# Optimization experiments

Hardware: AMD Instinct MI355X
Metric: run time of the kernel (lower is better)

Reference implementation:

```python
import jax, jax.numpy as jnp
import numpy as np

N_NODES = 100000
FEAT = 256
EMBED = 128
K = 10          # sampled neighbors per node (num_sample)
E = 4096        # edge batch
NUM_CLASSES = 2


def setup_inputs() -> dict:
    key = jax.random.key(0)
    ks = jax.random.split(key, 6)
    edges = jax.random.randint(ks[0], (E, 2), 0, N_NODES)
    neigh_idx = jax.random.randint(ks[1], (N_NODES, K), 0, N_NODES)
    features = jax.random.normal(ks[2], (N_NODES, FEAT), dtype=jnp.float32)
    W1 = jax.random.normal(ks[3], (EMBED, FEAT), dtype=jnp.float32) * (FEAT ** -0.5)
    W2 = jax.random.normal(ks[4], (EMBED, EMBED), dtype=jnp.float32) * (EMBED ** -0.5)
    Wc = jax.random.normal(ks[5], (NUM_CLASSES, EMBED), dtype=jnp.float32) * (EMBED ** -0.5)
    return {"edges": edges, "neigh_idx": neigh_idx, "features": features,
            "W1": W1, "W2": W2, "Wc": Wc}


def reference(edges, neigh_idx, features, W1, W2, Wc):
    # 2-layer GraphSage-style encoder (gcn mean aggregation), batched over E edges.
    idx2 = neigh_idx[edges]              # [E,2,K]   1-hop neighbors of edge endpoints
    idx1 = neigh_idx[idx2]               # [E,2,K,K] 2-hop neighbors
    # layer 1: mean of raw features over 2-hop neighbor sets, then linear + relu
    f1 = jnp.mean(features[idx1], axis=3)                 # [E,2,K,FEAT]
    h1 = jax.nn.relu(jnp.einsum('epkf,df->epkd', f1, W1)) # [E,2,K,EMBED]
    # layer 2: mean over 1-hop neighbors, then linear (last encoder: no relu)
    h1m = jnp.mean(h1, axis=2)                            # [E,2,EMBED]
    h2 = jnp.einsum('epd,gd->epg', h1m, W2)               # [E,2,EMBED]
    # edge pooling ('mean'): average the two endpoint embeddings
    pooled = 0.5 * (h2[:, 0] + h2[:, 1])                  # [E,EMBED]
    # classifier: weight.mm(embeds).t()
    return pooled @ Wc.T                                  # [E,NUM_CLASSES]
```

## Files before the change

kernel.cpp:

```cpp
#include <hip/hip_runtime.h>
#include <hip/hip_bf16.h>


typedef __bf16 bf16x8 __attribute__((ext_vector_type(8)));
typedef float f32x4 __attribute__((ext_vector_type(4)));

#define FEAT 256
#define EMB  128
#define KNB  10
#define BM   128

__device__ inline unsigned short f2b(float f) {
  unsigned int u = __float_as_uint(f);
  unsigned int r = (u + 0x7fffu + ((u >> 16) & 1u)) >> 16;
  return (unsigned short)r;
}
__device__ inline float b2f(unsigned int s) {
  return __uint_as_float(s << 16);
}


__global__ __launch_bounds__(512, 4) void gemm_z(
    const float* __restrict__ feat, const float* __restrict__ W1,
    const float* __restrict__ W2, const float* __restrict__ Wc,
    unsigned short* __restrict__ z, float* __restrict__ M2, int M) {
  __shared__ unsigned short As[BM][FEAT + 8];

  if (blockIdx.x == gridDim.x - 1) {
    int t = threadIdx.x;
    if (t < 256) {
      int c = t >> 7, d = t & 127;
      float s = 0.f;
      for (int g = 0; g < EMB; ++g) s += Wc[c * EMB + g] * W2[g * EMB + d];
      M2[t] = s;
    }
    return;
  }

  const int wid  = threadIdx.x >> 6;
  const int lane = threadIdx.x & 63;
  const int m0   = blockIdx.x * BM;

  bf16x8 bfrag[8];
  {
    const int col = wid * 16 + (lane & 15);
    const int kof = (lane >> 4) * 8;
#pragma unroll
    for (int kk = 0; kk < 8; ++kk) {
      const float* src = &W1[col * FEAT + kk * 32 + kof];
      float4 lo = *reinterpret_cast<const float4*>(src);
      float4 hi = *reinterpret_cast<const float4*>(src + 4);
      union { unsigned short s[8]; bf16x8 v; } cvt;
      cvt.s[0] = f2b(lo.x); cvt.s[1] = f2b(lo.y); cvt.s[2] = f2b(lo.z); cvt.s[3] = f2b(lo.w);
      cvt.s[4] = f2b(hi.x); cvt.s[5] = f2b(hi.y); cvt.s[6] = f2b(hi.z); cvt.s[7] = f2b(hi.w);
      bfrag[kk] = cvt.v;
    }
  }

  const float4* f4 = reinterpret_cast<const float4*>(feat);
  for (int i = threadIdx.x; i < BM * 64; i += 512) {
    int r = i >> 6, c4 = i & 63;
    int row = m0 + r;
    float4 v = make_float4(0.f, 0.f, 0.f, 0.f);
    if (row < M) v = f4[(size_t)row * 64 + c4];
    ushort4 bq;
    bq.x = f2b(v.x); bq.y = f2b(v.y); bq.z = f2b(v.z); bq.w = f2b(v.w);
    *reinterpret_cast<ushort4*>(&As[r][c4 * 4]) = bq;
  }
  __syncthreads();

  f32x4 acc[BM / 16] = {};
  const int arow = lane & 15;
  const int kof  = (lane >> 4) * 8;
#pragma unroll
  for (int mt = 0; mt < BM / 16; ++mt) {
#pragma unroll
    for (int kk = 0; kk < 8; ++kk) {
      bf16x8 a = *reinterpret_cast<const bf16x8*>(&As[mt * 16 + arow][kk * 32 + kof]);
      acc[mt] = __builtin_amdgcn_mfma_f32_16x16x32_bf16(a, bfrag[kk], acc[mt], 0, 0, 0);
    }
  }

  const int col = wid * 16 + (lane & 15);
#pragma unroll
  for (int mt = 0; mt < BM / 16; ++mt) {
    int rbase = m0 + mt * 16 + (lane >> 4) * 4;
#pragma unroll
    for (int r = 0; r < 4; ++r) {
      int row = rbase + r;
      if (row < M) z[(size_t)row * EMB + col] = f2b(acc[mt][r]);
    }
  }
}


__global__ __launch_bounds__(128) void aggregate(
    const int* __restrict__ edges, const int* __restrict__ nidx,
    const unsigned short* __restrict__ z, const float* __restrict__ M2,
    float* __restrict__ out, int E) {
  __shared__ int   s_idx2[2][KNB];
  __shared__ int   s_idx1[2][KNB * KNB];
  __shared__ float s_pm[2][EMB];

  const int e = blockIdx.x;
  const int t = threadIdx.x;
  const int w = t >> 6;
  const int l = t & 63;
  const int h = l >> 5;
  const int q = l & 31;

  if (t < 2 * KNB) {
    int p = t / KNB, k = t % KNB;
    int v = edges[e * 2 + p];
    s_idx2[p][k] = nidx[(size_t)v * KNB + k];
  }
  __syncthreads();
  for (int i = t; i < 2 * KNB * KNB; i += 128) {
    int p = i / 100, r = i % 100;
    s_idx1[p][r] = nidx[(size_t)s_idx2[p][r / KNB] * KNB + (r % KNB)];
  }
  __syncthreads();

  float pooled[4] = {0.f, 0.f, 0.f, 0.f};
#pragma unroll
  for (int k = 0; k < KNB; ++k) {
    float a[4] = {0.f, 0.f, 0.f, 0.f};
#pragma unroll
    for (int jp = 0; jp < KNB / 2; ++jp) {
      int u = s_idx1[w][k * KNB + jp * 2 + h];
      uint2 v = *reinterpret_cast<const uint2*>(&z[(size_t)u * EMB + q * 4]);
      a[0] += b2f(v.x & 0xffffu); a[1] += b2f(v.x >> 16);
      a[2] += b2f(v.y & 0xffffu); a[3] += b2f(v.y >> 16);
    }
#pragma unroll
    for (int c = 0; c < 4; ++c) {
      float s = a[c] + __shfl_xor(a[c], 32);
      pooled[c] += fmaxf(s * 0.1f, 0.f);
    }
  }
  if (h == 0) {
#pragma unroll
    for (int c = 0; c < 4; ++c) s_pm[w][q * 4 + c] = pooled[c] * 0.1f;
  }
  __syncthreads();

  if (w == 0) {
    int d0 = 2 * l, d1 = 2 * l + 1;
    float p0 = 0.5f * (s_pm[0][d0] + s_pm[1][d0]);
    float p1 = 0.5f * (s_pm[0][d1] + s_pm[1][d1]);
    float s0 = p0 * M2[d0]       + p1 * M2[d1];
    float s1 = p0 * M2[EMB + d0] + p1 * M2[EMB + d1];
#pragma unroll
    for (int off = 32; off > 0; off >>= 1) {
      s0 += __shfl_down(s0, off);
      s1 += __shfl_down(s1, off);
    }
    if (l == 0) { out[e * 2 + 0] = s0; out[e * 2 + 1] = s1; }
  }
}


extern "C" void kernel_launch(void* const* d_in, const int* in_sizes, int n_in,
                              void* d_out, int out_size, void* d_ws, size_t ws_size,
                              hipStream_t stream) {
  const int*   edges = (const int*)d_in[0];
  const int*   nidx  = (const int*)d_in[1];
  const float* feat  = (const float*)d_in[2];
  const float* W1    = (const float*)d_in[3];
  const float* W2    = (const float*)d_in[4];
  const float* Wc    = (const float*)d_in[5];
  float* out = (float*)d_out;

  const int N = in_sizes[2] / FEAT;
  const int E = in_sizes[0] / 2;

  char* ws = (char*)d_ws;
  unsigned short* z = (unsigned short*)ws;
  float* M2 = (float*)(ws + (size_t)N * EMB * sizeof(unsigned short));

  int mtiles = (N + BM - 1) / BM;
  gemm_z <<<mtiles + 1, 512, 0, stream>>>(feat, W1, W2, Wc, z, M2, N);
  aggregate<<<E, 128, 0, stream>>>(edges, nidx, z, M2, out, E);
}
```

Before: 211.2 us.

## Pre-convert features and W1 to swizzled bf16, load tiles via async global-to-LDS

Adds a separate conversion kernel that writes features (XOR-swizzled by row) and W1 as bf16 into workspace and computes the Wc·W2 product. The GEMM then pulls its A tile straight into LDS with global_load_lds and reads it with a matching swizzle, using a smaller 64-row tile. The aim is to remove conversion work and register staging from the GEMM and avoid LDS bank conflicts, but it adds a full bf16 write and re-read of the feature matrix plus an extra launch.

```diff
diff --git a/kernel.cpp b/kernel.cpp
--- a/kernel.cpp
+++ b/kernel.cpp
@@ -8,7 +8,7 @@
 #define FEAT 256
 #define EMB  128
 #define KNB  10
-#define BM   128
+#define BM   64
 
 __device__ inline unsigned short f2b(float f) {
   unsigned int u = __float_as_uint(f);
@@ -19,72 +19,99 @@
   return __uint_as_float(s << 16);
 }
 
-
-__global__ __launch_bounds__(512, 4) void gemm_z(
+__device__ __forceinline__ void async_ld16(unsigned short* lds, const unsigned short* g) {
+  __builtin_amdgcn_global_load_lds(
+      (const __attribute__((address_space(1))) unsigned int*)g,
+      (__attribute__((address_space(3))) unsigned int*)lds, 16, 0, 0);
+}
+
+
+__global__ __launch_bounds__(256) void fcvt(
     const float* __restrict__ feat, const float* __restrict__ W1,
     const float* __restrict__ W2, const float* __restrict__ Wc,
-    unsigned short* __restrict__ z, float* __restrict__ M2, int M) {
-  __shared__ unsigned short As[BM][FEAT + 8];
-
-  if (blockIdx.x == gridDim.x - 1) {
-    int t = threadIdx.x;
-    if (t < 256) {
-      int c = t >> 7, d = t & 127;
-      float s = 0.f;
-      for (int g = 0; g < EMB; ++g) s += Wc[c * EMB + g] * W2[g * EMB + d];
-      M2[t] = s;
-    }
-    return;
-  }
+    unsigned short* __restrict__ fb16, unsigned short* __restrict__ w1b,
+    float* __restrict__ M2, int N, int nbF) {
+  const int b = blockIdx.x;
+  const int t = threadIdx.x;
+
+  if (b < nbF) {
+    int g = b * 256 + t;
+    int r = g >> 5;
+    int s = g & 31;
+    float4 lo = make_float4(0.f, 0.f, 0.f, 0.f), hi = lo;
+    if (r < N) {
+      const float4* src = reinterpret_cast<const float4*>(&feat[(size_t)r * FEAT + s * 8]);
+      lo = src[0]; hi = src[1];
+    }
+    ushort4 a, c;
+    a.x = f2b(lo.x); a.y = f2b(lo.y); a.z = f2b(lo.z); a.w = f2b(lo.w);
+    c.x = f2b(hi.x); c.y = f2b(hi.y); c.z = f2b(hi.z); c.w = f2b(hi.w);
+    int sp = s ^ (r & 7);
+    ushort4* dst = reinterpret_cast<ushort4*>(&fb16[(size_t)r * FEAT + sp * 8]);
+    dst[0] = a; dst[1] = c;
+  } else if (b < nbF + 16) {
+    int g = (b - nbF) * 256 + t;
+    const float4* src = reinterpret_cast<const float4*>(&W1[g * 8]);
+    float4 lo = src[0], hi = src[1];
+    ushort4 a, c;
+    a.x = f2b(lo.x); a.y = f2b(lo.y); a.z = f2b(lo.z); a.w = f2b(lo.w);
+    c.x = f2b(hi.x); c.y = f2b(hi.y); c.z = f2b(hi.z); c.w = f2b(hi.w);
+    ushort4* dst = reinterpret_cast<ushort4*>(&w1b[g * 8]);
+    dst[0] = a; dst[1] = c;
+  } else {
+    int c = t >> 7, d = t & 127;
+    float s = 0.f;
+    for (int g = 0; g < EMB; ++g) s += Wc[c * EMB + g] * W2[g * EMB + d];
+    M2[t] = s;
+  }
+}
+
+
+__global__ __launch_bounds__(512, 4) void gemm_z(
+    const unsigned short* __restrict__ fb16, const unsigned short* __restrict__ w1b,
+    unsigned short* __restrict__ z, int M) {
+  __shared__ unsigned short As[BM * FEAT];
 
   const int wid  = threadIdx.x >> 6;
   const int lane = threadIdx.x & 63;
   const int m0   = blockIdx.x * BM;
 
+  const int col = wid * 16 + (lane & 15);
+  const int kof = (lane >> 4) * 8;
   bf16x8 bfrag[8];
+#pragma unroll
+  for (int kk = 0; kk < 8; ++kk)
+    bfrag[kk] = *reinterpret_cast<const bf16x8*>(&w1b[col * FEAT + kk * 32 + kof]);
+
   {
-    const int col = wid * 16 + (lane & 15);
-    const int kof = (lane >> 4) * 8;
-#pragma unroll
-    for (int kk = 0; kk < 8; ++kk) {
-      const float* src = &W1[col * FEAT + kk * 32 + kof];
-      float4 lo = *reinterpret_cast<const float4*>(src);
-      float4 hi = *reinterpret_cast<const float4*>(src + 4);
-      union { unsigned short s[8]; bf16x8 v; } cvt;
-      cvt.s[0] = f2b(lo.x); cvt.s[1] = f2b(lo.y); cvt.s[2] = f2b(lo.z); cvt.s[3] = f2b(lo.w);
-      cvt.s[4] = f2b(hi.x); cvt.s[5] = f2b(hi.y); cvt.s[6] = f2b(hi.z); cvt.s[7] = f2b(hi.w);
-      bfrag[kk] = cvt.v;
-    }
-  }
-
-  const float4* f4 = reinterpret_cast<const float4*>(feat);
-  for (int i = threadIdx.x; i < BM * 64; i += 512) {
-    int r = i >> 6, c4 = i & 63;
-    int row = m0 + r;
-    float4 v = make_float4(0.f, 0.f, 0.f, 0.f);
-    if (row < M) v = f4[(size_t)row * 64 + c4];
-    ushort4 bq;
-    bq.x = f2b(v.x); bq.y = f2b(v.y); bq.z = f2b(v.z); bq.w = f2b(v.w);
-    *reinterpret_cast<ushort4*>(&As[r][c4 * 4]) = bq;
+    const unsigned short* gbase = fb16 + (size_t)m0 * FEAT;
+#pragma unroll
+    for (int rnd = 0; rnd < 4; ++rnd) {
+      int off = rnd * 4096 + wid * 512;
+      async_ld16(&As[off], &gbase[off + lane * 8]);
+    }
   }
   __syncthreads();
 
   f32x4 acc[BM / 16] = {};
   const int arow = lane & 15;
-  const int kof  = (lane >> 4) * 8;
+  const int q    = lane >> 4;
 #pragma unroll
   for (int mt = 0; mt < BM / 16; ++mt) {
+    const int row = mt * 16 + arow;
+    const int rb  = row * FEAT;
+    const int rx  = row & 7;
 #pragma unroll
     for (int kk = 0; kk < 8; ++kk) {
-      bf16x8 a = *reinterpret_cast<const bf16x8*>(&As[mt * 16 + arow][kk * 32 + kof]);
+      int slot = (kk * 4 + q) ^ rx;
+      bf16x8 a = *reinterpret_cast<const bf16x8*>(&As[rb + slot * 8]);
       acc[mt] = __builtin_amdgcn_mfma_f32_16x16x32_bf16(a, bfrag[kk], acc[mt], 0, 0, 0);
     }
   }
 
-  const int col = wid * 16 + (lane & 15);
 #pragma unroll
   for (int mt = 0; mt < BM / 16; ++mt) {
-    int rbase = m0 + mt * 16 + (lane >> 4) * 4;
+    int rbase = m0 + mt * 16 + q * 4;
 #pragma unroll
     for (int r = 0; r < 4; ++r) {
       int row = rbase + r;
@@ -174,11 +201,17 @@
   const int N = in_sizes[2] / FEAT;
   const int E = in_sizes[0] / 2;
 
+  const int mtiles = (N + BM - 1) / BM;
+  const int NPAD   = mtiles * BM;
+
   char* ws = (char*)d_ws;
-  unsigned short* z = (unsigned short*)ws;
-  float* M2 = (float*)(ws + (size_t)N * EMB * sizeof(unsigned short));
-
-  int mtiles = (N + BM - 1) / BM;
-  gemm_z <<<mtiles + 1, 512, 0, stream>>>(feat, W1, W2, Wc, z, M2, N);
+  unsigned short* z    = (unsigned short*)ws;
+  unsigned short* fb16 = z + (size_t)N * EMB;
+  unsigned short* w1b  = fb16 + (size_t)NPAD * FEAT;
+  float*          M2   = (float*)(w1b + EMB * FEAT);
+
+  const int nbF = NPAD / 8;
+  fcvt     <<<nbF + 16 + 1, 256, 0, stream>>>(feat, W1, W2, Wc, fb16, w1b, M2, N, nbF);
+  gemm_z   <<<mtiles, 512, 0, stream>>>(fb16, w1b, z, N);
   aggregate<<<E, 128, 0, stream>>>(edges, nidx, z, M2, out, E);
 }
```

New measurement: 217.9 us. +3.2%, slower.
